# Performance work log

Measured on AMD Instinct MI355X. Metric: run time of the kernel, lower is better.

Reference implementation:

```python
import jax, jax.numpy as jnp
import numpy as np

N_NODES, N_EDGES, EMB_DIM = 100000, 1000000, 64
NUM_BOND_TYPE, NUM_BOND_DIR = 6, 3  # self-loop bond type index = 4


def gcn_conv(x, src, dst, bond_type, bond_dir, W, b, emb_bond, emb_dir):
    """One GCNConv (Hu et al. mol-GNN variant). src/dst/attrs already include self-loops."""
    N = x.shape[0]
    edge_emb = emb_bond[bond_type] + emb_dir[bond_dir]           # [Etot, D]
    ones = jnp.ones(src.shape[0], x.dtype)
    deg = jax.ops.segment_sum(ones, src, num_segments=N)         # scatter_add over row
    dis = jnp.where(deg > 0, jax.lax.rsqrt(deg), 0.0)
    norm = dis[src] * dis[dst]                                   # [Etot]
    h = x @ W.T + b                                              # [N, D]
    msg = norm[:, None] * (h[src] + edge_emb)                    # [Etot, D]
    return jax.ops.segment_sum(msg, dst, num_segments=N)         # add-aggregate at target


def with_self_loops(edge_index, edge_attr, N):
    loop = jnp.arange(N, dtype=edge_index.dtype)
    src = jnp.concatenate([edge_index[0], loop])
    dst = jnp.concatenate([edge_index[1], loop])
    bt = jnp.concatenate([edge_attr[:, 0], jnp.full((N,), 4, edge_attr.dtype)])
    bd = jnp.concatenate([edge_attr[:, 1], jnp.zeros((N,), edge_attr.dtype)])
    return src, dst, bt, bd


def setup_inputs() -> dict:
    key = jax.random.key(0)
    ks = jax.random.split(key, 12)
    D = EMB_DIM
    s = 1.0 / np.sqrt(D)
    inp = {
        "x": jax.random.normal(ks[0], (N_NODES, D), jnp.float32),
        "edge_index": jax.random.randint(ks[1], (2, N_EDGES), 0, N_NODES, jnp.int64 if jax.config.jax_enable_x64 else jnp.int32),
        "edge_attr": jax.random.randint(ks[2], (N_EDGES, 2), 0, 3, jnp.int64 if jax.config.jax_enable_x64 else jnp.int32),
        "W1": jax.random.uniform(ks[3], (D, D), jnp.float32, -s, s),
        "b1": jax.random.uniform(ks[4], (D,), jnp.float32, -s, s),
        "ebond1": jax.random.normal(ks[5], (NUM_BOND_TYPE, D), jnp.float32) * 0.1,
        "edir1": jax.random.normal(ks[6], (NUM_BOND_DIR, D), jnp.float32) * 0.1,
        "W2": jax.random.uniform(ks[7], (D, D), jnp.float32, -s, s),
        "b2": jax.random.uniform(ks[8], (D,), jnp.float32, -s, s),
        "ebond2": jax.random.normal(ks[9], (NUM_BOND_TYPE, D), jnp.float32) * 0.1,
        "edir2": jax.random.normal(ks[10], (NUM_BOND_DIR, D), jnp.float32) * 0.1,
    }
    return inp


def reference(x, edge_index, edge_attr, W1, b1, ebond1, edir1, W2, b2, ebond2, edir2):
    N = x.shape[0]
    src, dst, bt, bd = with_self_loops(edge_index, edge_attr, N)
    h = gcn_conv(x, src, dst, bt, bd, W1, b1, ebond1, edir1)
    h = jax.nn.relu(h)
    out = gcn_conv(h, src, dst, bt, bd, W2, b2, ebond2, edir2)
    return out
```

## Files before the change

kernel.cpp:

```cpp
#include <hip/hip_runtime.h>


#define THREADS 256
#define NBINS 512
#define BCAP 4096
#define CHUNK 2048
#define GEMM_SMEM_BYTES (64 * 68 * 4)
#define SC_SMEM (CHUNK * 4 * 2 + CHUNK * 2 * 2 + 6 * NBINS * 4 + 256 * 4)

typedef __attribute__((ext_vector_type(8))) short bf16x8;
typedef __attribute__((ext_vector_type(4))) float f32x4;

__device__ __forceinline__ float bflo(unsigned int v) { return __uint_as_float(v << 16); }
__device__ __forceinline__ float bfhi(unsigned int v) { return __uint_as_float(v & 0xFFFF0000u); }
__device__ __forceinline__ unsigned short f2bf(float f) {
    unsigned int u = __float_as_uint(f);
    return (unsigned short)((u + 0x7FFFu + ((u >> 16) & 1u)) >> 16);
}
__device__ __forceinline__ int sb(unsigned int w, int j) {
    return (int)(w << (24 - 8 * j)) >> 24;
}

__device__ __forceinline__ void load_bfrags(const float* __restrict__ W, int l15, int lk,
                                            bf16x8 bfr[4][2]) {
#pragma unroll
    for (int n = 0; n < 4; ++n) {
        const float* wp = W + (size_t)(16 * n + l15) * 64 + 8 * lk;
#pragma unroll
        for (int ks = 0; ks < 2; ++ks) {
            float4 u0 = *(const float4*)(wp + 32 * ks);
            float4 u1 = *(const float4*)(wp + 32 * ks + 4);
            bf16x8 bb;
            bb[0] = (short)f2bf(u0.x); bb[1] = (short)f2bf(u0.y);
            bb[2] = (short)f2bf(u0.z); bb[3] = (short)f2bf(u0.w);
            bb[4] = (short)f2bf(u1.x); bb[5] = (short)f2bf(u1.y);
            bb[6] = (short)f2bf(u1.z); bb[7] = (short)f2bf(u1.w);
            bfr[n][ks] = bb;
        }
    }
}

__device__ __forceinline__ void gemm_epilogue(int tile, f32x4 acc[4],
                                              const float* __restrict__ B, int wave,
                                              int l15, int lk, int t,
                                              unsigned short* __restrict__ Hb,
                                              unsigned char* __restrict__ Hq,
                                              float2* __restrict__ dscy,
                                              const float2* __restrict__ dsrc,
                                              float2* __restrict__ dsc2, int N,
                                              float (*smem)[68]) {
#pragma unroll
    for (int n = 0; n < 4; ++n) {
        float bv = B[16 * n + l15];
        int col = 16 * n + l15;
#pragma unroll
        for (int r = 0; r < 4; ++r)
            smem[16 * wave + 4 * lk + r][col] = acc[n][r] + bv;
    }
    __syncthreads();

#pragma unroll
    for (int i = 0; i < 2; ++i) {
        int idx = t + i * THREADS;
        int r = idx >> 3;
        int c8 = (idx & 7) << 3;
        int grow = tile * 64 + r;
        float4 va = *(const float4*)(&smem[r][c8]);
        float4 vb = *(const float4*)(&smem[r][c8 + 4]);
        float v[8] = {va.x, va.y, va.z, va.w, vb.x, vb.y, vb.z, vb.w};
        float m = fabsf(v[0]);
#pragma unroll
        for (int j = 1; j < 8; ++j) m = fmaxf(m, fabsf(v[j]));
        m = fmaxf(m, __shfl_xor(m, 1));
        m = fmaxf(m, __shfl_xor(m, 2));
        m = fmaxf(m, __shfl_xor(m, 4));
        if (grow < N) {
            uint4 o;
            o.x = (unsigned)f2bf(v[0]) | ((unsigned)f2bf(v[1]) << 16);
            o.y = (unsigned)f2bf(v[2]) | ((unsigned)f2bf(v[3]) << 16);
            o.z = (unsigned)f2bf(v[4]) | ((unsigned)f2bf(v[5]) << 16);
            o.w = (unsigned)f2bf(v[6]) | ((unsigned)f2bf(v[7]) << 16);
            *(uint4*)(Hb + (size_t)grow * 64 + c8) = o;
            float inv = m > 0.0f ? 127.0f / m : 0.0f;
            int q[8];
#pragma unroll
            for (int j = 0; j < 8; ++j) q[j] = __float2int_rn(v[j] * inv);
            uint2 qp;
            qp.x = (unsigned)(q[0] & 255) | ((unsigned)(q[1] & 255) << 8) |
                   ((unsigned)(q[2] & 255) << 16) | ((unsigned)(q[3] & 255) << 24);
            qp.y = (unsigned)(q[4] & 255) | ((unsigned)(q[5] & 255) << 8) |
                   ((unsigned)(q[6] & 255) << 16) | ((unsigned)(q[7] & 255) << 24);
            *(uint2*)(Hq + (size_t)grow * 64 + c8) = qp;
            if ((idx & 7) == 0) {
                float sc = m * (1.0f / 127.0f);
                if (dsc2) dsc2[grow] = make_float2(dsrc[grow].x, sc);
                else dscy[grow].y = sc;
            }
        }
    }
}

__device__ __forceinline__ void gemm64_body(int tile, const float* __restrict__ Xv,
                                            const float* __restrict__ W,
                                            const float* __restrict__ B,
                                            unsigned short* __restrict__ Hb,
                                            unsigned char* __restrict__ Hq,
                                            float2* __restrict__ dsc, int N,
                                            float (*smem)[68]) {
    int t = threadIdx.x;
    int lane = t & 63;
    int wave = __builtin_amdgcn_readfirstlane(t >> 6);
    int l15 = lane & 15;
    int lk = lane >> 4;
    int arow = tile * 64 + wave * 16 + l15;

    bf16x8 a0, a1;
    if (arow < N) {
        const float* xp = Xv + (size_t)arow * 64 + 8 * lk;
        float4 v0 = *(const float4*)xp;
        float4 v1 = *(const float4*)(xp + 4);
        float4 v2 = *(const float4*)(xp + 32);
        float4 v3 = *(const float4*)(xp + 36);
        a0[0] = (short)f2bf(v0.x); a0[1] = (short)f2bf(v0.y);
        a0[2] = (short)f2bf(v0.z); a0[3] = (short)f2bf(v0.w);
        a0[4] = (short)f2bf(v1.x); a0[5] = (short)f2bf(v1.y);
        a0[6] = (short)f2bf(v1.z); a0[7] = (short)f2bf(v1.w);
        a1[0] = (short)f2bf(v2.x); a1[1] = (short)f2bf(v2.y);
        a1[2] = (short)f2bf(v2.z); a1[3] = (short)f2bf(v2.w);
        a1[4] = (short)f2bf(v3.x); a1[5] = (short)f2bf(v3.y);
        a1[6] = (short)f2bf(v3.z); a1[7] = (short)f2bf(v3.w);
    } else {
#pragma unroll
        for (int e = 0; e < 8; ++e) { a0[e] = 0; a1[e] = 0; }
    }

    bf16x8 bfr[4][2];
    load_bfrags(W, l15, lk, bfr);

    f32x4 acc[4];
#pragma unroll
    for (int n = 0; n < 4; ++n) {
        f32x4 z = {0.0f, 0.0f, 0.0f, 0.0f};
        z = __builtin_amdgcn_mfma_f32_16x16x32_bf16(a0, bfr[n][0], z, 0, 0, 0);
        acc[n] = __builtin_amdgcn_mfma_f32_16x16x32_bf16(a1, bfr[n][1], z, 0, 0, 0);
    }
    gemm_epilogue(tile, acc, B, wave, l15, lk, t, Hb, Hq, dsc, nullptr, nullptr, N, smem);
}

__global__ __launch_bounds__(THREADS) void zero_gemm_kernel(
    int* __restrict__ gcur, int ncur, const float* __restrict__ X,
    const float* __restrict__ W1, const float* __restrict__ B1,
    unsigned short* __restrict__ Hb, unsigned char* __restrict__ Hq,
    float2* __restrict__ dsc, int N, int tile0) {
    __shared__ __align__(16) char sh[GEMM_SMEM_BYTES];
    int b = blockIdx.x;
    if (b == 0) {
        for (int i = threadIdx.x; i < ncur; i += THREADS) gcur[i] = 0;
        return;
    }
    gemm64_body(tile0 + b - 1, X, W1, B1, Hb, Hq, dsc, N, (float(*)[68])sh);
}

__global__ __launch_bounds__(THREADS) void scatter_kernel(
    const int* __restrict__ src, const int* __restrict__ dst, const int* __restrict__ attr,
    int* __restrict__ gcurS, int* __restrict__ gcurD, unsigned char* __restrict__ payS,
    unsigned int* __restrict__ payD, int E, int SCB,
    const float* __restrict__ X, const float* __restrict__ W1, const float* __restrict__ B1,
    unsigned short* __restrict__ Hb, unsigned char* __restrict__ Hq,
    float2* __restrict__ dsc, int N, int tile0) {
    __shared__ __align__(16) char sh[SC_SMEM];
    int b = blockIdx.x;
    if (b >= SCB) {
        gemm64_body(tile0 + b - SCB, X, W1, B1, Hb, Hq, dsc, N, (float(*)[68])sh);
        return;
    }
    unsigned int* Wv = (unsigned int*)sh;
    unsigned int* SD = Wv + CHUNK;
    unsigned short* DB = (unsigned short*)(SD + CHUNK);
    unsigned short* SDB = DB + CHUNK;
    int* hD = (int*)(SDB + CHUNK);
    int* hS = hD + NBINS;
    int* mapD = hS + NBINS;
    int* mapS = mapD + NBINS;
    int* curD = mapS + NBINS;
    int* curS = curD + NBINS;
    int* scn = curS + NBINS;
    unsigned char* SS = (unsigned char*)Wv;
    unsigned short* SSB = DB;

    int t = threadIdx.x;
    for (int k = t; k < NBINS; k += THREADS) { hD[k] = 0; hS[k] = 0; }
    __syncthreads();

    int lo = b * CHUNK, hi = min(E, lo + CHUNK);
    int nch = hi - lo;
    const int2* ap = (const int2*)attr;
    for (int li = t; li < nch; li += THREADS) {
        int i = lo + li;
        int sv = src[i], dv = dst[i];
        int2 a = ap[i];
        Wv[li] = (unsigned int)sv | ((unsigned int)(a.x * 3 + a.y) << 17) |
                 ((unsigned int)(dv & 255) << 22);
        DB[li] = (unsigned short)(dv >> 8);
        atomicAdd(&hD[dv >> 8], 1);
        atomicAdd(&hS[sv >> 8], 1);
    }
    __syncthreads();

    for (int k = t; k < NBINS; k += THREADS) {
        int h = hD[k];
        int r = h ? atomicAdd(&gcurD[k], h) : 0;
        mapD[k] = k * BCAP + r;
        int h2 = hS[k];
        int r2 = h2 ? atomicAdd(&gcurS[k], h2) : 0;
        mapS[k] = k * BCAP + r2;
    }
    __syncthreads();

    scn[t] = hD[2 * t] + hD[2 * t + 1];
    __syncthreads();
    for (int d = 1; d < THREADS; d <<= 1) {
        int a = (t >= d) ? scn[t - d] : 0;
        __syncthreads();
        scn[t] += a;
        __syncthreads();
    }
    {
        int off = t ? scn[t - 1] : 0;
        curD[2 * t] = off;
        curD[2 * t + 1] = off + hD[2 * t];
        mapD[2 * t] -= off;
        mapD[2 * t + 1] -= off + hD[2 * t];
    }
    __syncthreads();
    scn[t] = hS[2 * t] + hS[2 * t + 1];
    __syncthreads();
    for (int d = 1; d < THREADS; d <<= 1) {
        int a = (t >= d) ? scn[t - d] : 0;
        __syncthreads();
        scn[t] += a;
        __syncthreads();
    }
    {
        int off = t ? scn[t - 1] : 0;
        curS[2 * t] = off;
        curS[2 * t + 1] = off + hS[2 * t];
        mapS[2 * t] -= off;
        mapS[2 * t + 1] -= off + hS[2 * t];
    }
    __syncthreads();

    for (int li = t; li < nch; li += THREADS) {
        int k = DB[li];
        int p = atomicAdd(&curD[k], 1);
        SD[p] = Wv[li];
        SDB[p] = (unsigned short)k;
    }
    __syncthreads();

    for (int li = t; li < nch; li += THREADS) {
        int val = (int)(SD[li] & 0x1FFFFu);
        int k = val >> 8;
        int p = atomicAdd(&curS[k], 1);
        SS[p] = (unsigned char)(val & 255);
        SSB[p] = (unsigned short)k;
    }
    __syncthreads();

    for (int li = t; li < nch; li += THREADS) {
        payD[mapD[SDB[li]] + li] = SD[li];
        payS[mapS[SSB[li]] + li] = SS[li];
    }
}

__global__ __launch_bounds__(THREADS) void build_kernel(
    const unsigned char* __restrict__ payS, const unsigned int* __restrict__ payD,
    const int* __restrict__ gcurS, const int* __restrict__ gcurD,
    unsigned int* __restrict__ sorted, int2* __restrict__ rc,
    int NB2, float2* __restrict__ dsc, int N) {
    __shared__ int cnt[256];
    __shared__ int cur[256];
    __shared__ int s[THREADS];
    int t = threadIdx.x;
    int b = blockIdx.x;
    if (b < NB2) {
        int k = b;
        cnt[t] = 0;
        __syncthreads();
        int n = gcurS[k], off = k * BCAP;
        for (int i = t; i < n; i += THREADS) atomicAdd(&cnt[payS[off + i]], 1);
        __syncthreads();
        int node = k * 256 + t;
        if (node < N) dsc[node].x = 1.0f / sqrtf(1.0f + (float)cnt[t]);
    } else {
        int k = b - NB2;
        cnt[t] = 0;
        __syncthreads();
        int ecnt = gcurD[k], eoff = k * BCAP;
        for (int i = t; i < ecnt; i += THREADS)
            atomicAdd(&cnt[(payD[eoff + i] >> 22) & 255], 1);
        __syncthreads();
        int v = cnt[t];
        s[t] = v;
        __syncthreads();
        for (int d = 1; d < THREADS; d <<= 1) {
            int a = (t >= d) ? s[t - d] : 0;
            __syncthreads();
            s[t] += a;
            __syncthreads();
        }
        int excl = s[t] - v;
        int node = k * 256 + t;
        if (node < N) rc[node] = make_int2(eoff + excl, v);
        cur[t] = excl;
        __syncthreads();
        for (int i = t; i < ecnt; i += THREADS) {
            unsigned int u = payD[eoff + i];
            int p = atomicAdd(&cur[(u >> 22) & 255], 1);
            sorted[eoff + p] = u & 0x3FFFFFu;
        }
    }
}

__device__ __forceinline__ void edge_acc(unsigned int u, float dn,
                                         const float2* __restrict__ dsc,
                                         const unsigned char* __restrict__ Hq, int c,
                                         const float (*embc)[64], float acc[8]) {
    int s0 = u & 0x1FFFF;
    int e0 = (u >> 17) & 31;
    float2 ds = dsc[s0];
    uint2 q = *(const uint2*)(Hq + (size_t)s0 * 64 + c);
    float w = ds.x * dn, ws = w * ds.y;
    float4 ea = *(const float4*)(&embc[e0][c]);
    float4 eb = *(const float4*)(&embc[e0][c + 4]);
    acc[0] = fmaf(ws, (float)sb(q.x, 0), fmaf(w, ea.x, acc[0]));
    acc[1] = fmaf(ws, (float)sb(q.x, 1), fmaf(w, ea.y, acc[1]));
    acc[2] = fmaf(ws, (float)sb(q.x, 2), fmaf(w, ea.z, acc[2]));
    acc[3] = fmaf(ws, (float)sb(q.x, 3), fmaf(w, ea.w, acc[3]));
    acc[4] = fmaf(ws, (float)sb(q.y, 0), fmaf(w, eb.x, acc[4]));
    acc[5] = fmaf(ws, (float)sb(q.y, 1), fmaf(w, eb.y, acc[5]));
    acc[6] = fmaf(ws, (float)sb(q.y, 2), fmaf(w, eb.z, acc[6]));
    acc[7] = fmaf(ws, (float)sb(q.y, 3), fmaf(w, eb.w, acc[7]));
}

__device__ __forceinline__ void agg_node(int n, int c, const unsigned short* __restrict__ Hb,
                                         const unsigned char* __restrict__ Hq,
                                         const float2* __restrict__ dsc,
                                         const int2* __restrict__ rc,
                                         const unsigned int* __restrict__ entries,
                                         const float (*ec)[64], float o[8]) {
    float dn = dsc[n].x;
    uint4 hv = *(const uint4*)(Hb + (size_t)n * 64 + c);
    float4 ea = *(const float4*)(&ec[12][c]);
    float4 eb = *(const float4*)(&ec[12][c + 4]);
    float nrm = dn * dn;
    float accA[8], accB[8];
    accA[0] = nrm * (bflo(hv.x) + ea.x);
    accA[1] = nrm * (bfhi(hv.x) + ea.y);
    accA[2] = nrm * (bflo(hv.y) + ea.z);
    accA[3] = nrm * (bfhi(hv.y) + ea.w);
    accA[4] = nrm * (bflo(hv.z) + eb.x);
    accA[5] = nrm * (bfhi(hv.z) + eb.y);
    accA[6] = nrm * (bflo(hv.w) + eb.z);
    accA[7] = nrm * (bfhi(hv.w) + eb.w);
#pragma unroll
    for (int j = 0; j < 8; ++j) accB[j] = 0.0f;

    int2 pc = rc[n];
    int p = pc.x;
    int end = p + pc.y;
    for (; p + 3 < end; p += 4) {
        unsigned int u0 = entries[p];
        unsigned int u1 = entries[p + 1];
        unsigned int u2 = entries[p + 2];
        unsigned int u3 = entries[p + 3];
        edge_acc(u0, dn, dsc, Hq, c, ec, accA);
        edge_acc(u1, dn, dsc, Hq, c, ec, accB);
        edge_acc(u2, dn, dsc, Hq, c, ec, accA);
        edge_acc(u3, dn, dsc, Hq, c, ec, accB);
    }
    for (; p < end; ++p) edge_acc(entries[p], dn, dsc, Hq, c, ec, accA);
#pragma unroll
    for (int j = 0; j < 8; ++j) o[j] = accA[j] + accB[j];
}

__global__ __launch_bounds__(THREADS) void agg_gemm_kernel(
    const unsigned short* __restrict__ Hb1, const unsigned char* __restrict__ Hq1,
    const float2* __restrict__ dsc, const float* __restrict__ ebond,
    const float* __restrict__ edir, const int2* __restrict__ rc,
    const unsigned int* __restrict__ entries, const float* __restrict__ W,
    const float* __restrict__ B, unsigned short* __restrict__ Hb2,
    unsigned char* __restrict__ Hq2, float2* __restrict__ dsc2, int N) {
    __shared__ float embc[18][64];
    __shared__ __align__(16) unsigned short smA[64][72];
    __shared__ __align__(16) float smC[64][68];
    int t = threadIdx.x;
    for (int i = t; i < 18 * 64; i += THREADS) {
        int row = i >> 6, c = i & 63;
        embc[row][c] = ebond[(row / 3) * 64 + c] + edir[(row % 3) * 64 + c];
    }
    __syncthreads();

    int tile = blockIdx.x;
    const float(*ec)[64] = (const float(*)[64])embc;
#pragma unroll 1
    for (int r = 0; r < 2; ++r) {
        int ln = r * 32 + (t >> 3);
        int n = tile * 64 + ln;
        int c = (t & 7) << 3;
        uint4 ov = make_uint4(0u, 0u, 0u, 0u);
        if (n < N) {
            float o[8];
            agg_node(n, c, Hb1, Hq1, dsc, rc, entries, ec, o);
            ov.x = (unsigned)f2bf(fmaxf(o[0], 0.0f)) | ((unsigned)f2bf(fmaxf(o[1], 0.0f)) << 16);
            ov.y = (unsigned)f2bf(fmaxf(o[2], 0.0f)) | ((unsigned)f2bf(fmaxf(o[3], 0.0f)) << 16);
            ov.z = (unsigned)f2bf(fmaxf(o[4], 0.0f)) | ((unsigned)f2bf(fmaxf(o[5], 0.0f)) << 16);
            ov.w = (unsigned)f2bf(fmaxf(o[6], 0.0f)) | ((unsigned)f2bf(fmaxf(o[7], 0.0f)) << 16);
        }
        *(uint4*)(&smA[ln][c]) = ov;
    }
    __syncthreads();

    int lane = t & 63;
    int wave = __builtin_amdgcn_readfirstlane(t >> 6);
    int l15 = lane & 15;
    int lk = lane >> 4;
    int lrow = wave * 16 + l15;
    bf16x8 a0 = *(const bf16x8*)(&smA[lrow][8 * lk]);
    bf16x8 a1 = *(const bf16x8*)(&smA[lrow][8 * lk + 32]);

    bf16x8 bfr[4][2];
    load_bfrags(W, l15, lk, bfr);

    f32x4 acc[4];
#pragma unroll
    for (int n = 0; n < 4; ++n) {
        f32x4 z = {0.0f, 0.0f, 0.0f, 0.0f};
        z = __builtin_amdgcn_mfma_f32_16x16x32_bf16(a0, bfr[n][0], z, 0, 0, 0);
        acc[n] = __builtin_amdgcn_mfma_f32_16x16x32_bf16(a1, bfr[n][1], z, 0, 0, 0);
    }
    gemm_epilogue(tile, acc, B, wave, l15, lk, t, Hb2, Hq2, nullptr, dsc, dsc2, N, smC);
}

__global__ __launch_bounds__(THREADS) void aggregate_kernel(
    const unsigned short* __restrict__ Hb, const unsigned char* __restrict__ Hq,
    const float2* __restrict__ dsc, const float* __restrict__ ebond,
    const float* __restrict__ edir, const int2* __restrict__ rc,
    const unsigned int* __restrict__ entries, float* __restrict__ out, int N) {
    __shared__ float embc[18][64];
    int t = threadIdx.x;
    for (int i = t; i < 18 * 64; i += THREADS) {
        int row = i >> 6, c = i & 63;
        embc[row][c] = ebond[(row / 3) * 64 + c] + edir[(row % 3) * 64 + c];
    }
    __syncthreads();

    int n = blockIdx.x * 32 + (t >> 3);
    if (n >= N) return;
    int c = (t & 7) << 3;
    float o[8];
    agg_node(n, c, Hb, Hq, dsc, rc, entries, (const float(*)[64])embc, o);
    *(float4*)(out + (size_t)n * 64 + c) = make_float4(o[0], o[1], o[2], o[3]);
    *(float4*)(out + (size_t)n * 64 + c + 4) = make_float4(o[4], o[5], o[6], o[7]);
}

extern "C" void kernel_launch(void* const* d_in, const int* in_sizes, int n_in,
                              void* d_out, int out_size, void* d_ws, size_t ws_size,
                              hipStream_t stream) {
    const float* x      = (const float*)d_in[0];
    const int*   eidx   = (const int*)d_in[1];
    const int*   eattr  = (const int*)d_in[2];
    const float* W1     = (const float*)d_in[3];
    const float* b1     = (const float*)d_in[4];
    const float* ebond1 = (const float*)d_in[5];
    const float* edir1  = (const float*)d_in[6];
    const float* W2     = (const float*)d_in[7];
    const float* b2     = (const float*)d_in[8];
    const float* ebond2 = (const float*)d_in[9];
    const float* edir2  = (const float*)d_in[10];

    const int N = in_sizes[0] / 64;
    const int E = in_sizes[1] / 2;
    const int* src = eidx;
    const int* dst = eidx + E;
    float* out = (float*)d_out;
    const int NB2 = (N + 255) >> 8;
    const int SCB = (E + CHUNK - 1) / CHUNK;

    char* w = (char*)d_ws;
    size_t Na = ((size_t)N * 4 + 255) & ~(size_t)255;
    float2* dsc    = (float2*)w;           w += 2 * Na;
    float2* dsc2   = (float2*)w;           w += 2 * Na;
    int2*  rc      = (int2*)w;             w += 2 * Na;
    int*   gcur    = (int*)w;              w += 2 * NBINS * 4;
    unsigned int* payD   = (unsigned int*)w;   w += (size_t)NBINS * BCAP * 4;
    unsigned int* sorted = (unsigned int*)w;   w += (size_t)NBINS * BCAP * 4;
    unsigned char* payS  = (unsigned char*)w;  w += (size_t)NBINS * BCAP;
    unsigned short* Hb1  = (unsigned short*)w; w += (size_t)N * 64 * 2;
    unsigned char*  Hq1  = (unsigned char*)w;  w += ((size_t)N * 64 + 255) & ~(size_t)255;
    unsigned short* Hb2  = (unsigned short*)w; w += (size_t)N * 64 * 2;
    unsigned char*  Hq2  = (unsigned char*)w;  w += ((size_t)N * 64 + 255) & ~(size_t)255;
    int* gcurS = gcur;
    int* gcurD = gcur + NBINS;

    const int gT   = (N + 63) / 64;
    const int gN32 = (N + 31) / 32;

    const int t0 = min(gT, 512);
    const int t1 = gT - t0;

    zero_gemm_kernel<<<1 + t0, THREADS, 0, stream>>>(gcur, 2 * NBINS, x, W1, b1, Hb1, Hq1,
                                                     dsc, N, 0);
    scatter_kernel<<<SCB + t1, THREADS, 0, stream>>>(src, dst, eattr, gcurS, gcurD, payS,
                                                     payD, E, SCB, x, W1, b1, Hb1, Hq1,
                                                     dsc, N, t0);
    build_kernel<<<2 * NB2, THREADS, 0, stream>>>(payS, payD, gcurS, gcurD, sorted,
                                                  rc, NB2, dsc, N);

    agg_gemm_kernel<<<gT, THREADS, 0, stream>>>(Hb1, Hq1, dsc, ebond1, edir1, rc, sorted,
                                                W2, b2, Hb2, Hq2, dsc2, N);

    aggregate_kernel<<<gN32, THREADS, 0, stream>>>(Hb2, Hq2, dsc2, ebond2, edir2, rc,
                                                   sorted, out, N);
}
```

Baseline: 220.3 us.

## Factor edge-embedding term into per-node coefficients and prefold source scale

The edge-embedding contribution is now taken out of the per-edge loop. For each destination node, the sum of source norms per bond type and per direction is precomputed once during the sort pass. The aggregation then rebuilds the embedding term from six coefficients and a small table, shared by both layers. The per-source dis*scale product is folded into one float array, so the inner edge loop does one gather and eight FMAs instead of two. In exchange the build is split into two kernels (adding a launch), shared-memory float atomics are added in the sort, and 32 bytes per node of coefficients are written and read.

Measured after the change: 230.7 us. 4.7% more time.

```diff
diff --git a/kernel.cpp b/kernel.cpp
--- a/kernel.cpp
+++ b/kernel.cpp
@@ -45,9 +45,8 @@
                                               int l15, int lk, int t,
                                               unsigned short* __restrict__ Hb,
                                               unsigned char* __restrict__ Hq,
-                                              float2* __restrict__ dscy,
-                                              const float2* __restrict__ dsrc,
-                                              float2* __restrict__ dsc2, int N,
+                                              float* __restrict__ scout,
+                                              const float* __restrict__ dismul, int N,
                                               float (*smem)[68]) {
 #pragma unroll
     for (int n = 0; n < 4; ++n) {
@@ -93,8 +92,7 @@
             *(uint2*)(Hq + (size_t)grow * 64 + c8) = qp;
             if ((idx & 7) == 0) {
                 float sc = m * (1.0f / 127.0f);
-                if (dsc2) dsc2[grow] = make_float2(dsrc[grow].x, sc);
-                else dscy[grow].y = sc;
+                scout[grow] = dismul ? dismul[grow] * sc : sc;
             }
         }
     }
@@ -105,7 +103,7 @@
                                             const float* __restrict__ B,
                                             unsigned short* __restrict__ Hb,
                                             unsigned char* __restrict__ Hq,
-                                            float2* __restrict__ dsc, int N,
+                                            float* __restrict__ sc1, int N,
                                             float (*smem)[68]) {
     int t = threadIdx.x;
     int lane = t & 63;
@@ -144,21 +142,21 @@
         z = __builtin_amdgcn_mfma_f32_16x16x32_bf16(a0, bfr[n][0], z, 0, 0, 0);
         acc[n] = __builtin_amdgcn_mfma_f32_16x16x32_bf16(a1, bfr[n][1], z, 0, 0, 0);
     }
-    gemm_epilogue(tile, acc, B, wave, l15, lk, t, Hb, Hq, dsc, nullptr, nullptr, N, smem);
+    gemm_epilogue(tile, acc, B, wave, l15, lk, t, Hb, Hq, sc1, nullptr, N, smem);
 }
 
 __global__ __launch_bounds__(THREADS) void zero_gemm_kernel(
     int* __restrict__ gcur, int ncur, const float* __restrict__ X,
     const float* __restrict__ W1, const float* __restrict__ B1,
     unsigned short* __restrict__ Hb, unsigned char* __restrict__ Hq,
-    float2* __restrict__ dsc, int N, int tile0) {
+    float* __restrict__ sc1, int N, int tile0) {
     __shared__ __align__(16) char sh[GEMM_SMEM_BYTES];
     int b = blockIdx.x;
     if (b == 0) {
         for (int i = threadIdx.x; i < ncur; i += THREADS) gcur[i] = 0;
         return;
     }
-    gemm64_body(tile0 + b - 1, X, W1, B1, Hb, Hq, dsc, N, (float(*)[68])sh);
+    gemm64_body(tile0 + b - 1, X, W1, B1, Hb, Hq, sc1, N, (float(*)[68])sh);
 }
 
 __global__ __launch_bounds__(THREADS) void scatter_kernel(
@@ -167,11 +165,11 @@
     unsigned int* __restrict__ payD, int E, int SCB,
     const float* __restrict__ X, const float* __restrict__ W1, const float* __restrict__ B1,
     unsigned short* __restrict__ Hb, unsigned char* __restrict__ Hq,
-    float2* __restrict__ dsc, int N, int tile0) {
+    float* __restrict__ sc1, int N, int tile0) {
     __shared__ __align__(16) char sh[SC_SMEM];
     int b = blockIdx.x;
     if (b >= SCB) {
-        gemm64_body(tile0 + b - SCB, X, W1, B1, Hb, Hq, dsc, N, (float(*)[68])sh);
+        gemm64_body(tile0 + b - SCB, X, W1, B1, Hb, Hq, sc1, N, (float(*)[68])sh);
         return;
     }
     unsigned int* Wv = (unsigned int*)sh;
@@ -273,86 +271,106 @@
     }
 }
 
-__global__ __launch_bounds__(THREADS) void build_kernel(
-    const unsigned char* __restrict__ payS, const unsigned int* __restrict__ payD,
-    const int* __restrict__ gcurS, const int* __restrict__ gcurD,
+__global__ __launch_bounds__(THREADS) void build_deg_kernel(
+    const unsigned char* __restrict__ payS, const int* __restrict__ gcurS,
+    float* __restrict__ disv, int N) {
+    __shared__ int cnt[256];
+    int t = threadIdx.x;
+    int k = blockIdx.x;
+    cnt[t] = 0;
+    __syncthreads();
+    int n = gcurS[k], off = k * BCAP;
+    for (int i = t; i < n; i += THREADS) atomicAdd(&cnt[payS[off + i]], 1);
+    __syncthreads();
+    int node = k * 256 + t;
+    if (node < N) disv[node] = 1.0f / sqrtf(1.0f + (float)cnt[t]);
+}
+
+__global__ __launch_bounds__(THREADS) void build_sort_kernel(
+    const unsigned int* __restrict__ payD, const int* __restrict__ gcurD,
     unsigned int* __restrict__ sorted, int2* __restrict__ rc,
-    int NB2, float2* __restrict__ dsc, int N) {
+    const float* __restrict__ disv, const float* __restrict__ sc1,
+    float* __restrict__ coefv, float* __restrict__ g1, int N) {
     __shared__ int cnt[256];
     __shared__ int cur[256];
     __shared__ int s[THREADS];
-    int t = threadIdx.x;
-    int b = blockIdx.x;
-    if (b < NB2) {
-        int k = b;
-        cnt[t] = 0;
+    __shared__ float coefL[256][8];
+    int t = threadIdx.x;
+    int k = blockIdx.x;
+    cnt[t] = 0;
+#pragma unroll
+    for (int j = 0; j < 8; ++j) coefL[t][j] = 0.0f;
+    __syncthreads();
+    int ecnt = gcurD[k], eoff = k * BCAP;
+    for (int i = t; i < ecnt; i += THREADS)
+        atomicAdd(&cnt[(payD[eoff + i] >> 22) & 255], 1);
+    __syncthreads();
+    int v = cnt[t];
+    s[t] = v;
+    __syncthreads();
+    for (int d = 1; d < THREADS; d <<= 1) {
+        int a = (t >= d) ? s[t - d] : 0;
         __syncthreads();
-        int n = gcurS[k], off = k * BCAP;
-        for (int i = t; i < n; i += THREADS) atomicAdd(&cnt[payS[off + i]], 1);
+        s[t] += a;
         __syncthreads();
-        int node = k * 256 + t;
-        if (node < N) dsc[node].x = 1.0f / sqrtf(1.0f + (float)cnt[t]);
-    } else {
-        int k = b - NB2;
-        cnt[t] = 0;
-        __syncthreads();
-        int ecnt = gcurD[k], eoff = k * BCAP;
-        for (int i = t; i < ecnt; i += THREADS)
-            atomicAdd(&cnt[(payD[eoff + i] >> 22) & 255], 1);
-        __syncthreads();
-        int v = cnt[t];
-        s[t] = v;
-        __syncthreads();
-        for (int d = 1; d < THREADS; d <<= 1) {
-            int a = (t >= d) ? s[t - d] : 0;
-            __syncthreads();
-            s[t] += a;
-            __syncthreads();
-        }
-        int excl = s[t] - v;
-        int node = k * 256 + t;
-        if (node < N) rc[node] = make_int2(eoff + excl, v);
-        cur[t] = excl;
-        __syncthreads();
-        for (int i = t; i < ecnt; i += THREADS) {
-            unsigned int u = payD[eoff + i];
-            int p = atomicAdd(&cur[(u >> 22) & 255], 1);
-            sorted[eoff + p] = u & 0x3FFFFFu;
-        }
+    }
+    int excl = s[t] - v;
+    int node = k * 256 + t;
+    if (node < N) rc[node] = make_int2(eoff + excl, v);
+    cur[t] = excl;
+    __syncthreads();
+    for (int i = t; i < ecnt; i += THREADS) {
+        unsigned int u = payD[eoff + i];
+        int d8 = (u >> 22) & 255;
+        int p = atomicAdd(&cur[d8], 1);
+        sorted[eoff + p] = u & 0x3FFFFFu;
+        int s0 = u & 0x1FFFF;
+        int e = (u >> 17) & 31;
+        int bt = (e >= 6) ? 2 : ((e >= 3) ? 1 : 0);
+        int bd = e - 3 * bt;
+        float dv = disv[s0];
+        atomicAdd(&coefL[d8][bt], dv);
+        atomicAdd(&coefL[d8][4 + bd], dv);
+    }
+    __syncthreads();
+    if (node < N) {
+        float4 c0 = make_float4(coefL[t][0], coefL[t][1], coefL[t][2], coefL[t][4]);
+        float4 c1 = make_float4(coefL[t][5], coefL[t][6], 0.0f, 0.0f);
+        *(float4*)(coefv + 8 * (size_t)node) = c0;
+        *(float4*)(coefv + 8 * (size_t)node + 4) = c1;
+        g1[node] = disv[node] * sc1[node];
     }
 }
 
 __device__ __forceinline__ void edge_acc(unsigned int u, float dn,
-                                         const float2* __restrict__ dsc,
+                                         const float* __restrict__ g,
                                          const unsigned char* __restrict__ Hq, int c,
-                                         const float (*embc)[64], float acc[8]) {
+                                         float acc[8]) {
     int s0 = u & 0x1FFFF;
-    int e0 = (u >> 17) & 31;
-    float2 ds = dsc[s0];
+    float w = dn * g[s0];
     uint2 q = *(const uint2*)(Hq + (size_t)s0 * 64 + c);
-    float w = ds.x * dn, ws = w * ds.y;
-    float4 ea = *(const float4*)(&embc[e0][c]);
-    float4 eb = *(const float4*)(&embc[e0][c + 4]);
-    acc[0] = fmaf(ws, (float)sb(q.x, 0), fmaf(w, ea.x, acc[0]));
-    acc[1] = fmaf(ws, (float)sb(q.x, 1), fmaf(w, ea.y, acc[1]));
-    acc[2] = fmaf(ws, (float)sb(q.x, 2), fmaf(w, ea.z, acc[2]));
-    acc[3] = fmaf(ws, (float)sb(q.x, 3), fmaf(w, ea.w, acc[3]));
-    acc[4] = fmaf(ws, (float)sb(q.y, 0), fmaf(w, eb.x, acc[4]));
-    acc[5] = fmaf(ws, (float)sb(q.y, 1), fmaf(w, eb.y, acc[5]));
-    acc[6] = fmaf(ws, (float)sb(q.y, 2), fmaf(w, eb.z, acc[6]));
-    acc[7] = fmaf(ws, (float)sb(q.y, 3), fmaf(w, eb.w, acc[7]));
+    acc[0] = fmaf(w, (float)sb(q.x, 0), acc[0]);
+    acc[1] = fmaf(w, (float)sb(q.x, 1), acc[1]);
+    acc[2] = fmaf(w, (float)sb(q.x, 2), acc[2]);
+    acc[3] = fmaf(w, (float)sb(q.x, 3), acc[3]);
+    acc[4] = fmaf(w, (float)sb(q.y, 0), acc[4]);
+    acc[5] = fmaf(w, (float)sb(q.y, 1), acc[5]);
+    acc[6] = fmaf(w, (float)sb(q.y, 2), acc[6]);
+    acc[7] = fmaf(w, (float)sb(q.y, 3), acc[7]);
 }
 
 __device__ __forceinline__ void agg_node(int n, int c, const unsigned short* __restrict__ Hb,
                                          const unsigned char* __restrict__ Hq,
-                                         const float2* __restrict__ dsc,
+                                         const float* __restrict__ disv,
+                                         const float* __restrict__ g,
+                                         const float* __restrict__ coefv,
                                          const int2* __restrict__ rc,
                                          const unsigned int* __restrict__ entries,
-                                         const float (*ec)[64], float o[8]) {
-    float dn = dsc[n].x;
+                                         const float (*et)[64], float o[8]) {
+    float dn = disv[n];
     uint4 hv = *(const uint4*)(Hb + (size_t)n * 64 + c);
-    float4 ea = *(const float4*)(&ec[12][c]);
-    float4 eb = *(const float4*)(&ec[12][c + 4]);
+    float4 ea = *(const float4*)(&et[6][c]);
+    float4 eb = *(const float4*)(&et[6][c + 4]);
     float nrm = dn * dn;
     float accA[8], accB[8];
     accA[0] = nrm * (bflo(hv.x) + ea.x);
@@ -374,35 +392,57 @@
         unsigned int u1 = entries[p + 1];
         unsigned int u2 = entries[p + 2];
         unsigned int u3 = entries[p + 3];
-        edge_acc(u0, dn, dsc, Hq, c, ec, accA);
-        edge_acc(u1, dn, dsc, Hq, c, ec, accB);
-        edge_acc(u2, dn, dsc, Hq, c, ec, accA);
-        edge_acc(u3, dn, dsc, Hq, c, ec, accB);
-    }
-    for (; p < end; ++p) edge_acc(entries[p], dn, dsc, Hq, c, ec, accA);
-#pragma unroll
-    for (int j = 0; j < 8; ++j) o[j] = accA[j] + accB[j];
+        edge_acc(u0, dn, g, Hq, c, accA);
+        edge_acc(u1, dn, g, Hq, c, accB);
+        edge_acc(u2, dn, g, Hq, c, accA);
+        edge_acc(u3, dn, g, Hq, c, accB);
+    }
+    for (; p < end; ++p) edge_acc(entries[p], dn, g, Hq, c, accA);
+
+    float4 c0 = *(const float4*)(coefv + 8 * (size_t)n);
+    float4 c1 = *(const float4*)(coefv + 8 * (size_t)n + 4);
+#pragma unroll
+    for (int j = 0; j < 8; ++j) {
+        float e = c0.x * et[0][c + j];
+        e = fmaf(c0.y, et[1][c + j], e);
+        e = fmaf(c0.z, et[2][c + j], e);
+        e = fmaf(c0.w, et[3][c + j], e);
+        e = fmaf(c1.x, et[4][c + j], e);
+        e = fmaf(c1.y, et[5][c + j], e);
+        o[j] = fmaf(dn, e, accA[j] + accB[j]);
+    }
+}
+
+__device__ __forceinline__ void fill_et(float (*et)[64], const float* __restrict__ ebond,
+                                        const float* __restrict__ edir) {
+    int t = threadIdx.x;
+    for (int i = t; i < 7 * 64; i += THREADS) {
+        int row = i >> 6, c = i & 63;
+        float v;
+        if (row < 3) v = ebond[row * 64 + c];
+        else if (row < 6) v = edir[(row - 3) * 64 + c];
+        else v = ebond[4 * 64 + c] + edir[c];
+        et[row][c] = v;
+    }
 }
 
 __global__ __launch_bounds__(THREADS) void agg_gemm_kernel(
     const unsigned short* __restrict__ Hb1, const unsigned char* __restrict__ Hq1,
-    const float2* __restrict__ dsc, const float* __restrict__ ebond,
+    const float* __restrict__ disv, const float* __restrict__ g1,
+    const float* __restrict__ coefv, const float* __restrict__ ebond,
     const float* __restrict__ edir, const int2* __restrict__ rc,
     const unsigned int* __restrict__ entries, const float* __restrict__ W,
     const float* __restrict__ B, unsigned short* __restrict__ Hb2,
-    unsigned char* __restrict__ Hq2, float2* __restrict__ dsc2, int N) {
-    __shared__ float embc[18][64];
+    unsigned char* __restrict__ Hq2, float* __restrict__ g2, int N) {
+    __shared__ float et[7][64];
     __shared__ __align__(16) unsigned short smA[64][72];
     __shared__ __align__(16) float smC[64][68];
     int t = threadIdx.x;
-    for (int i = t; i < 18 * 64; i += THREADS) {
-        int row = i >> 6, c = i & 63;
-        embc[row][c] = ebond[(row / 3) * 64 + c] + edir[(row % 3) * 64 + c];
-    }
+    fill_et(et, ebond, edir);
     __syncthreads();
 
     int tile = blockIdx.x;
-    const float(*ec)[64] = (const float(*)[64])embc;
+    const float(*ec)[64] = (const float(*)[64])et;
 #pragma unroll 1
     for (int r = 0; r < 2; ++r) {
         int ln = r * 32 + (t >> 3);
@@ -411,7 +451,7 @@
         uint4 ov = make_uint4(0u, 0u, 0u, 0u);
         if (n < N) {
             float o[8];
-            agg_node(n, c, Hb1, Hq1, dsc, rc, entries, ec, o);
+            agg_node(n, c, Hb1, Hq1, disv, g1, coefv, rc, entries, ec, o);
             ov.x = (unsigned)f2bf(fmaxf(o[0], 0.0f)) | ((unsigned)f2bf(fmaxf(o[1], 0.0f)) << 16);
             ov.y = (unsigned)f2bf(fmaxf(o[2], 0.0f)) | ((unsigned)f2bf(fmaxf(o[3], 0.0f)) << 16);
             ov.z = (unsigned)f2bf(fmaxf(o[4], 0.0f)) | ((unsigned)f2bf(fmaxf(o[5], 0.0f)) << 16);
@@ -439,27 +479,25 @@
         z = __builtin_amdgcn_mfma_f32_16x16x32_bf16(a0, bfr[n][0], z, 0, 0, 0);
         acc[n] = __builtin_amdgcn_mfma_f32_16x16x32_bf16(a1, bfr[n][1], z, 0, 0, 0);
     }
-    gemm_epilogue(tile, acc, B, wave, l15, lk, t, Hb2, Hq2, nullptr, dsc, dsc2, N, smC);
+    gemm_epilogue(tile, acc, B, wave, l15, lk, t, Hb2, Hq2, g2, disv, N, smC);
 }
 
 __global__ __launch_bounds__(THREADS) void aggregate_kernel(
     const unsigned short* __restrict__ Hb, const unsigned char* __restrict__ Hq,
-    const float2* __restrict__ dsc, const float* __restrict__ ebond,
+    const float* __restrict__ disv, const float* __restrict__ g,
+    const float* __restrict__ coefv, const float* __restrict__ ebond,
     const float* __restrict__ edir, const int2* __restrict__ rc,
     const unsigned int* __restrict__ entries, float* __restrict__ out, int N) {
-    __shared__ float embc[18][64];
-    int t = threadIdx.x;
-    for (int i = t; i < 18 * 64; i += THREADS) {
-        int row = i >> 6, c = i & 63;
-        embc[row][c] = ebond[(row / 3) * 64 + c] + edir[(row % 3) * 64 + c];
-    }
+    __shared__ float et[7][64];
+    int t = threadIdx.x;
+    fill_et(et, ebond, edir);
     __syncthreads();
 
     int n = blockIdx.x * 32 + (t >> 3);
     if (n >= N) return;
     int c = (t & 7) << 3;
     float o[8];
-    agg_node(n, c, Hb, Hq, dsc, rc, entries, (const float(*)[64])embc, o);
+    agg_node(n, c, Hb, Hq, disv, g, coefv, rc, entries, (const float(*)[64])et, o);
     *(float4*)(out + (size_t)n * 64 + c) = make_float4(o[0], o[1], o[2], o[3]);
     *(float4*)(out + (size_t)n * 64 + c + 4) = make_float4(o[4], o[5], o[6], o[7]);
 }
@@ -489,8 +527,11 @@
 
     char* w = (char*)d_ws;
     size_t Na = ((size_t)N * 4 + 255) & ~(size_t)255;
-    float2* dsc    = (float2*)w;           w += 2 * Na;
-    float2* dsc2   = (float2*)w;           w += 2 * Na;
+    float* disv    = (float*)w;            w += Na;
+    float* sc1     = (float*)w;            w += Na;
+    float* g1      = (float*)w;            w += Na;
+    float* g2      = (float*)w;            w += Na;
+    float* coefv   = (float*)w;            w += 8 * Na;
     int2*  rc      = (int2*)w;             w += 2 * Na;
     int*   gcur    = (int*)w;              w += 2 * NBINS * 4;
     unsigned int* payD   = (unsigned int*)w;   w += (size_t)NBINS * BCAP * 4;
@@ -510,16 +551,17 @@
     const int t1 = gT - t0;
 
     zero_gemm_kernel<<<1 + t0, THREADS, 0, stream>>>(gcur, 2 * NBINS, x, W1, b1, Hb1, Hq1,
-                                                     dsc, N, 0);
+                                                     sc1, N, 0);
     scatter_kernel<<<SCB + t1, THREADS, 0, stream>>>(src, dst, eattr, gcurS, gcurD, payS,
                                                      payD, E, SCB, x, W1, b1, Hb1, Hq1,
-                                                     dsc, N, t0);
-    build_kernel<<<2 * NB2, THREADS, 0, stream>>>(payS, payD, gcurS, gcurD, sorted,
-                                                  rc, NB2, dsc, N);
-
-    agg_gemm_kernel<<<gT, THREADS, 0, stream>>>(Hb1, Hq1, dsc, ebond1, edir1, rc, sorted,
-                                                W2, b2, Hb2, Hq2, dsc2, N);
-
-    aggregate_kernel<<<gN32, THREADS, 0, stream>>>(Hb2, Hq2, dsc2, ebond2, edir2, rc,
-                                                   sorted, out, N);
-}
+                                                     sc1, N, t0);
+    build_deg_kernel<<<NB2, THREADS, 0, stream>>>(payS, gcurS, disv, N);
+    build_sort_kernel<<<NB2, THREADS, 0, stream>>>(payD, gcurD, sorted, rc, disv, sc1,
+                                                   coefv, g1, N);
+
+    agg_gemm_kernel<<<gT, THREADS, 0, stream>>>(Hb1, Hq1, disv, g1, coefv, ebond1, edir1,
+                                                rc, sorted, W2, b2, Hb2, Hq2, g2, N);
+
+    aggregate_kernel<<<gN32, THREADS, 0, stream>>>(Hb2, Hq2, disv, g2, coefv, ebond2,
+                                                   edir2, rc, sorted, out, N);
+}
```

## Pack int8 features with per-node norm and scale into 128-byte records

Applied to the files above, without the earlier changes.

The separate int8 feature array and float2 degree/scale array are merged into one 128-byte-per-node record: 64 bytes of quantized features, then dis and scale at offset 64. The per-edge gather in aggregation then touches a single record region instead of two separate arrays, aiming to cut scattered memory transactions. The cost is doubled record footprint with 56 padding bytes per node, and the degree value is now written into the record by the build kernel while the GEMM epilogue writes the scale.

Measured after the change: 222.6 us. No clear change (+1.0%).

```diff
diff --git a/kernel.cpp b/kernel.cpp
--- a/kernel.cpp
+++ b/kernel.cpp
@@ -44,10 +44,8 @@
                                               const float* __restrict__ B, int wave,
                                               int l15, int lk, int t,
                                               unsigned short* __restrict__ Hb,
-                                              unsigned char* __restrict__ Hq,
-                                              float2* __restrict__ dscy,
-                                              const float2* __restrict__ dsrc,
-                                              float2* __restrict__ dsc2, int N,
+                                              unsigned char* __restrict__ Hqr,
+                                              const float* __restrict__ dismul, int N,
                                               float (*smem)[68]) {
 #pragma unroll
     for (int n = 0; n < 4; ++n) {
@@ -90,11 +88,12 @@
                    ((unsigned)(q[2] & 255) << 16) | ((unsigned)(q[3] & 255) << 24);
             qp.y = (unsigned)(q[4] & 255) | ((unsigned)(q[5] & 255) << 8) |
                    ((unsigned)(q[6] & 255) << 16) | ((unsigned)(q[7] & 255) << 24);
-            *(uint2*)(Hq + (size_t)grow * 64 + c8) = qp;
+            unsigned char* rec = Hqr + (size_t)grow * 128;
+            *(uint2*)(rec + c8) = qp;
             if ((idx & 7) == 0) {
                 float sc = m * (1.0f / 127.0f);
-                if (dsc2) dsc2[grow] = make_float2(dsrc[grow].x, sc);
-                else dscy[grow].y = sc;
+                if (dismul) *(float2*)(rec + 64) = make_float2(dismul[grow], sc);
+                else *(float*)(rec + 68) = sc;
             }
         }
     }
@@ -104,8 +103,7 @@
                                             const float* __restrict__ W,
                                             const float* __restrict__ B,
                                             unsigned short* __restrict__ Hb,
-                                            unsigned char* __restrict__ Hq,
-                                            float2* __restrict__ dsc, int N,
+                                            unsigned char* __restrict__ Hqr, int N,
                                             float (*smem)[68]) {
     int t = threadIdx.x;
     int lane = t & 63;
@@ -144,21 +142,20 @@
         z = __builtin_amdgcn_mfma_f32_16x16x32_bf16(a0, bfr[n][0], z, 0, 0, 0);
         acc[n] = __builtin_amdgcn_mfma_f32_16x16x32_bf16(a1, bfr[n][1], z, 0, 0, 0);
     }
-    gemm_epilogue(tile, acc, B, wave, l15, lk, t, Hb, Hq, dsc, nullptr, nullptr, N, smem);
+    gemm_epilogue(tile, acc, B, wave, l15, lk, t, Hb, Hqr, nullptr, N, smem);
 }
 
 __global__ __launch_bounds__(THREADS) void zero_gemm_kernel(
     int* __restrict__ gcur, int ncur, const float* __restrict__ X,
     const float* __restrict__ W1, const float* __restrict__ B1,
-    unsigned short* __restrict__ Hb, unsigned char* __restrict__ Hq,
-    float2* __restrict__ dsc, int N, int tile0) {
+    unsigned short* __restrict__ Hb, unsigned char* __restrict__ Hqr, int N, int tile0) {
     __shared__ __align__(16) char sh[GEMM_SMEM_BYTES];
     int b = blockIdx.x;
     if (b == 0) {
         for (int i = threadIdx.x; i < ncur; i += THREADS) gcur[i] = 0;
         return;
     }
-    gemm64_body(tile0 + b - 1, X, W1, B1, Hb, Hq, dsc, N, (float(*)[68])sh);
+    gemm64_body(tile0 + b - 1, X, W1, B1, Hb, Hqr, N, (float(*)[68])sh);
 }
 
 __global__ __launch_bounds__(THREADS) void scatter_kernel(
@@ -166,12 +163,11 @@
     int* __restrict__ gcurS, int* __restrict__ gcurD, unsigned char* __restrict__ payS,
     unsigned int* __restrict__ payD, int E, int SCB,
     const float* __restrict__ X, const float* __restrict__ W1, const float* __restrict__ B1,
-    unsigned short* __restrict__ Hb, unsigned char* __restrict__ Hq,
-    float2* __restrict__ dsc, int N, int tile0) {
+    unsigned short* __restrict__ Hb, unsigned char* __restrict__ Hqr, int N, int tile0) {
     __shared__ __align__(16) char sh[SC_SMEM];
     int b = blockIdx.x;
     if (b >= SCB) {
-        gemm64_body(tile0 + b - SCB, X, W1, B1, Hb, Hq, dsc, N, (float(*)[68])sh);
+        gemm64_body(tile0 + b - SCB, X, W1, B1, Hb, Hqr, N, (float(*)[68])sh);
         return;
     }
     unsigned int* Wv = (unsigned int*)sh;
@@ -277,7 +273,7 @@
     const unsigned char* __restrict__ payS, const unsigned int* __restrict__ payD,
     const int* __restrict__ gcurS, const int* __restrict__ gcurD,
     unsigned int* __restrict__ sorted, int2* __restrict__ rc,
-    int NB2, float2* __restrict__ dsc, int N) {
+    float* __restrict__ disv, unsigned char* __restrict__ Hqr1, int NB2, int N) {
     __shared__ int cnt[256];
     __shared__ int cur[256];
     __shared__ int s[THREADS];
@@ -291,7 +287,11 @@
         for (int i = t; i < n; i += THREADS) atomicAdd(&cnt[payS[off + i]], 1);
         __syncthreads();
         int node = k * 256 + t;
-        if (node < N) dsc[node].x = 1.0f / sqrtf(1.0f + (float)cnt[t]);
+        if (node < N) {
+            float dv = 1.0f / sqrtf(1.0f + (float)cnt[t]);
+            disv[node] = dv;
+            *(float*)(Hqr1 + (size_t)node * 128 + 64) = dv;
+        }
     } else {
         int k = b - NB2;
         cnt[t] = 0;
@@ -323,13 +323,13 @@
 }
 
 __device__ __forceinline__ void edge_acc(unsigned int u, float dn,
-                                         const float2* __restrict__ dsc,
-                                         const unsigned char* __restrict__ Hq, int c,
+                                         const unsigned char* __restrict__ Hqr, int c,
                                          const float (*embc)[64], float acc[8]) {
     int s0 = u & 0x1FFFF;
     int e0 = (u >> 17) & 31;
-    float2 ds = dsc[s0];
-    uint2 q = *(const uint2*)(Hq + (size_t)s0 * 64 + c);
+    const unsigned char* rec = Hqr + (size_t)s0 * 128;
+    float2 ds = *(const float2*)(rec + 64);
+    uint2 q = *(const uint2*)(rec + c);
     float w = ds.x * dn, ws = w * ds.y;
     float4 ea = *(const float4*)(&embc[e0][c]);
     float4 eb = *(const float4*)(&embc[e0][c + 4]);
@@ -344,12 +344,12 @@
 }
 
 __device__ __forceinline__ void agg_node(int n, int c, const unsigned short* __restrict__ Hb,
-                                         const unsigned char* __restrict__ Hq,
-                                         const float2* __restrict__ dsc,
+                                         const unsigned char* __restrict__ Hqr,
+                                         const float* __restrict__ disv,
                                          const int2* __restrict__ rc,
                                          const unsigned int* __restrict__ entries,
                                          const float (*ec)[64], float o[8]) {
-    float dn = dsc[n].x;
+    float dn = disv[n];
     uint4 hv = *(const uint4*)(Hb + (size_t)n * 64 + c);
     float4 ea = *(const float4*)(&ec[12][c]);
     float4 eb = *(const float4*)(&ec[12][c + 4]);
@@ -374,23 +374,23 @@
         unsigned int u1 = entries[p + 1];
         unsigned int u2 = entries[p + 2];
         unsigned int u3 = entries[p + 3];
-        edge_acc(u0, dn, dsc, Hq, c, ec, accA);
-        edge_acc(u1, dn, dsc, Hq, c, ec, accB);
-        edge_acc(u2, dn, dsc, Hq, c, ec, accA);
-        edge_acc(u3, dn, dsc, Hq, c, ec, accB);
-    }
-    for (; p < end; ++p) edge_acc(entries[p], dn, dsc, Hq, c, ec, accA);
+        edge_acc(u0, dn, Hqr, c, ec, accA);
+        edge_acc(u1, dn, Hqr, c, ec, accB);
+        edge_acc(u2, dn, Hqr, c, ec, accA);
+        edge_acc(u3, dn, Hqr, c, ec, accB);
+    }
+    for (; p < end; ++p) edge_acc(entries[p], dn, Hqr, c, ec, accA);
 #pragma unroll
     for (int j = 0; j < 8; ++j) o[j] = accA[j] + accB[j];
 }
 
 __global__ __launch_bounds__(THREADS) void agg_gemm_kernel(
-    const unsigned short* __restrict__ Hb1, const unsigned char* __restrict__ Hq1,
-    const float2* __restrict__ dsc, const float* __restrict__ ebond,
+    const unsigned short* __restrict__ Hb1, const unsigned char* __restrict__ Hqr1,
+    const float* __restrict__ disv, const float* __restrict__ ebond,
     const float* __restrict__ edir, const int2* __restrict__ rc,
     const unsigned int* __restrict__ entries, const float* __restrict__ W,
     const float* __restrict__ B, unsigned short* __restrict__ Hb2,
-    unsigned char* __restrict__ Hq2, float2* __restrict__ dsc2, int N) {
+    unsigned char* __restrict__ Hqr2, int N) {
     __shared__ float embc[18][64];
     __shared__ __align__(16) unsigned short smA[64][72];
     __shared__ __align__(16) float smC[64][68];
@@ -411,7 +411,7 @@
         uint4 ov = make_uint4(0u, 0u, 0u, 0u);
         if (n < N) {
             float o[8];
-            agg_node(n, c, Hb1, Hq1, dsc, rc, entries, ec, o);
+            agg_node(n, c, Hb1, Hqr1, disv, rc, entries, ec, o);
             ov.x = (unsigned)f2bf(fmaxf(o[0], 0.0f)) | ((unsigned)f2bf(fmaxf(o[1], 0.0f)) << 16);
             ov.y = (unsigned)f2bf(fmaxf(o[2], 0.0f)) | ((unsigned)f2bf(fmaxf(o[3], 0.0f)) << 16);
             ov.z = (unsigned)f2bf(fmaxf(o[4], 0.0f)) | ((unsigned)f2bf(fmaxf(o[5], 0.0f)) << 16);
@@ -439,12 +439,12 @@
         z = __builtin_amdgcn_mfma_f32_16x16x32_bf16(a0, bfr[n][0], z, 0, 0, 0);
         acc[n] = __builtin_amdgcn_mfma_f32_16x16x32_bf16(a1, bfr[n][1], z, 0, 0, 0);
     }
-    gemm_epilogue(tile, acc, B, wave, l15, lk, t, Hb2, Hq2, nullptr, dsc, dsc2, N, smC);
+    gemm_epilogue(tile, acc, B, wave, l15, lk, t, Hb2, Hqr2, disv, N, smC);
 }
 
 __global__ __launch_bounds__(THREADS) void aggregate_kernel(
-    const unsigned short* __restrict__ Hb, const unsigned char* __restrict__ Hq,
-    const float2* __restrict__ dsc, const float* __restrict__ ebond,
+    const unsigned short* __restrict__ Hb, const unsigned char* __restrict__ Hqr,
+    const float* __restrict__ disv, const float* __restrict__ ebond,
     const float* __restrict__ edir, const int2* __restrict__ rc,
     const unsigned int* __restrict__ entries, float* __restrict__ out, int N) {
     __shared__ float embc[18][64];
@@ -459,7 +459,7 @@
     if (n >= N) return;
     int c = (t & 7) << 3;
     float o[8];
-    agg_node(n, c, Hb, Hq, dsc, rc, entries, (const float(*)[64])embc, o);
+    agg_node(n, c, Hb, Hqr, disv, rc, entries, (const float(*)[64])embc, o);
     *(float4*)(out + (size_t)n * 64 + c) = make_float4(o[0], o[1], o[2], o[3]);
     *(float4*)(out + (size_t)n * 64 + c + 4) = make_float4(o[4], o[5], o[6], o[7]);
 }
@@ -489,17 +489,17 @@
 
     char* w = (char*)d_ws;
     size_t Na = ((size_t)N * 4 + 255) & ~(size_t)255;
-    float2* dsc    = (float2*)w;           w += 2 * Na;
-    float2* dsc2   = (float2*)w;           w += 2 * Na;
+    size_t Nr = ((size_t)N * 128 + 255) & ~(size_t)255;
+    float* disv    = (float*)w;            w += Na;
     int2*  rc      = (int2*)w;             w += 2 * Na;
     int*   gcur    = (int*)w;              w += 2 * NBINS * 4;
     unsigned int* payD   = (unsigned int*)w;   w += (size_t)NBINS * BCAP * 4;
     unsigned int* sorted = (unsigned int*)w;   w += (size_t)NBINS * BCAP * 4;
     unsigned char* payS  = (unsigned char*)w;  w += (size_t)NBINS * BCAP;
     unsigned short* Hb1  = (unsigned short*)w; w += (size_t)N * 64 * 2;
-    unsigned char*  Hq1  = (unsigned char*)w;  w += ((size_t)N * 64 + 255) & ~(size_t)255;
+    unsigned char*  Hqr1 = (unsigned char*)w;  w += Nr;
     unsigned short* Hb2  = (unsigned short*)w; w += (size_t)N * 64 * 2;
-    unsigned char*  Hq2  = (unsigned char*)w;  w += ((size_t)N * 64 + 255) & ~(size_t)255;
+    unsigned char*  Hqr2 = (unsigned char*)w;  w += Nr;
     int* gcurS = gcur;
     int* gcurD = gcur + NBINS;
 
@@ -509,17 +509,17 @@
     const int t0 = min(gT, 512);
     const int t1 = gT - t0;
 
-    zero_gemm_kernel<<<1 + t0, THREADS, 0, stream>>>(gcur, 2 * NBINS, x, W1, b1, Hb1, Hq1,
-                                                     dsc, N, 0);
+    zero_gemm_kernel<<<1 + t0, THREADS, 0, stream>>>(gcur, 2 * NBINS, x, W1, b1, Hb1, Hqr1,
+                                                     N, 0);
     scatter_kernel<<<SCB + t1, THREADS, 0, stream>>>(src, dst, eattr, gcurS, gcurD, payS,
-                                                     payD, E, SCB, x, W1, b1, Hb1, Hq1,
-                                                     dsc, N, t0);
-    build_kernel<<<2 * NB2, THREADS, 0, stream>>>(payS, payD, gcurS, gcurD, sorted,
-                                                  rc, NB2, dsc, N);
-
-    agg_gemm_kernel<<<gT, THREADS, 0, stream>>>(Hb1, Hq1, dsc, ebond1, edir1, rc, sorted,
-                                                W2, b2, Hb2, Hq2, dsc2, N);
-
-    aggregate_kernel<<<gN32, THREADS, 0, stream>>>(Hb2, Hq2, dsc2, ebond2, edir2, rc,
+                                                     payD, E, SCB, x, W1, b1, Hb1, Hqr1,
+                                                     N, t0);
+    build_kernel<<<2 * NB2, THREADS, 0, stream>>>(payS, payD, gcurS, gcurD, sorted, rc,
+                                                  disv, Hqr1, NB2, N);
+
+    agg_gemm_kernel<<<gT, THREADS, 0, stream>>>(Hb1, Hqr1, disv, ebond1, edir1, rc, sorted,
+                                                W2, b2, Hb2, Hqr2, N);
+
+    aggregate_kernel<<<gN32, THREADS, 0, stream>>>(Hb2, Hqr2, disv, ebond2, edir2, rc,
                                                    sorted, out, N);
 }
```

## Move all layer-1 GEMM tiles into zero kernel and alias agg_gemm LDS buffers

Applied to the files above, without the earlier changes.

The layer-1 GEMM tiles that were split between the zero-init kernel and the tail of the scatter kernel now all run in the zero-init kernel, so the scatter kernel only does edge binning. Separately, agg_gemm_kernel overlays its bf16 A-tile and fp32 C-tile in a single shared-memory buffer, with an added barrier after the A fragments are read. The aliasing cuts LDS use per block and may allow more resident blocks. The cost is losing the overlap of GEMM work with scattering, plus one extra barrier.

Result: no change. 221.7 us (+0.6%).

```diff
diff --git a/kernel.cpp b/kernel.cpp
--- a/kernel.cpp
+++ b/kernel.cpp
@@ -151,29 +151,22 @@
     int* __restrict__ gcur, int ncur, const float* __restrict__ X,
     const float* __restrict__ W1, const float* __restrict__ B1,
     unsigned short* __restrict__ Hb, unsigned char* __restrict__ Hq,
-    float2* __restrict__ dsc, int N, int tile0) {
+    float2* __restrict__ dsc, int N) {
     __shared__ __align__(16) char sh[GEMM_SMEM_BYTES];
     int b = blockIdx.x;
     if (b == 0) {
         for (int i = threadIdx.x; i < ncur; i += THREADS) gcur[i] = 0;
         return;
     }
-    gemm64_body(tile0 + b - 1, X, W1, B1, Hb, Hq, dsc, N, (float(*)[68])sh);
+    gemm64_body(b - 1, X, W1, B1, Hb, Hq, dsc, N, (float(*)[68])sh);
 }
 
 __global__ __launch_bounds__(THREADS) void scatter_kernel(
     const int* __restrict__ src, const int* __restrict__ dst, const int* __restrict__ attr,
     int* __restrict__ gcurS, int* __restrict__ gcurD, unsigned char* __restrict__ payS,
-    unsigned int* __restrict__ payD, int E, int SCB,
-    const float* __restrict__ X, const float* __restrict__ W1, const float* __restrict__ B1,
-    unsigned short* __restrict__ Hb, unsigned char* __restrict__ Hq,
-    float2* __restrict__ dsc, int N, int tile0) {
+    unsigned int* __restrict__ payD, int E) {
     __shared__ __align__(16) char sh[SC_SMEM];
     int b = blockIdx.x;
-    if (b >= SCB) {
-        gemm64_body(tile0 + b - SCB, X, W1, B1, Hb, Hq, dsc, N, (float(*)[68])sh);
-        return;
-    }
     unsigned int* Wv = (unsigned int*)sh;
     unsigned int* SD = Wv + CHUNK;
     unsigned short* DB = (unsigned short*)(SD + CHUNK);
@@ -392,8 +385,9 @@
     const float* __restrict__ B, unsigned short* __restrict__ Hb2,
     unsigned char* __restrict__ Hq2, float2* __restrict__ dsc2, int N) {
     __shared__ float embc[18][64];
-    __shared__ __align__(16) unsigned short smA[64][72];
-    __shared__ __align__(16) float smC[64][68];
+    __shared__ __align__(16) char smU[64 * 68 * 4];
+    unsigned short (*smA)[72] = (unsigned short(*)[72])smU;
+    float (*smC)[68] = (float(*)[68])smU;
     int t = threadIdx.x;
     for (int i = t; i < 18 * 64; i += THREADS) {
         int row = i >> 6, c = i & 63;
@@ -428,6 +422,7 @@
     int lrow = wave * 16 + l15;
     bf16x8 a0 = *(const bf16x8*)(&smA[lrow][8 * lk]);
     bf16x8 a1 = *(const bf16x8*)(&smA[lrow][8 * lk + 32]);
+    __syncthreads();
 
     bf16x8 bfr[4][2];
     load_bfrags(W, l15, lk, bfr);
@@ -506,14 +501,10 @@
     const int gT   = (N + 63) / 64;
     const int gN32 = (N + 31) / 32;
 
-    const int t0 = min(gT, 512);
-    const int t1 = gT - t0;
-
-    zero_gemm_kernel<<<1 + t0, THREADS, 0, stream>>>(gcur, 2 * NBINS, x, W1, b1, Hb1, Hq1,
-                                                     dsc, N, 0);
-    scatter_kernel<<<SCB + t1, THREADS, 0, stream>>>(src, dst, eattr, gcurS, gcurD, payS,
-                                                     payD, E, SCB, x, W1, b1, Hb1, Hq1,
-                                                     dsc, N, t0);
+    zero_gemm_kernel<<<1 + gT, THREADS, 0, stream>>>(gcur, 2 * NBINS, x, W1, b1, Hb1, Hq1,
+                                                     dsc, N);
+    scatter_kernel<<<SCB, THREADS, 0, stream>>>(src, dst, eattr, gcurS, gcurD, payS,
+                                                payD, E);
     build_kernel<<<2 * NB2, THREADS, 0, stream>>>(payS, payD, gcurS, gcurD, sorted,
                                                   rc, NB2, dsc, N);
 
```
